# Optimization experiments

Measured on AMD Instinct MI355X. Metric: run time of the kernel, lower is better.

The kernel has to match this reference:

```python
import jax, jax.numpy as jnp
import numpy as np

ALPHA = 0.2  # LeakyReLU negative slope
NEG = -9e15

def _gat_head(Wh, a1, a2, adj_mask):
    # Wh: [N,O], a1/a2: [O], adj_mask: [N,N] bool
    e = jax.nn.leaky_relu(jnp.einsum('no,o->n', Wh, a1)[:, None]
                          + jnp.einsum('no,o->n', Wh, a2)[None, :], ALPHA)
    att = jax.nn.softmax(jnp.where(adj_mask, e, NEG), axis=-1)
    return att @ Wh  # [N,O]

def setup_inputs() -> dict:
    key = jax.random.key(0)
    ks = jax.random.split(key, 6)
    N, F_IN, O, H, C = 4096, 512, 64, 8, 16
    x = jax.random.normal(ks[0], (N, F_IN), jnp.float32)
    adj = jax.random.randint(ks[1], (N, N), 0, 2, jnp.int32)
    W = jax.random.normal(ks[2], (H, F_IN, O), jnp.float32) * 0.05
    a = jax.random.normal(ks[3], (H, 2 * O), jnp.float32) * 0.05
    W_out = jax.random.normal(ks[4], (H * O, C), jnp.float32) * 0.05
    a_out = jax.random.normal(ks[5], (2 * C,), jnp.float32) * 0.05
    return {'x': x, 'adj': adj, 'W': W, 'a': a, 'W_out': W_out, 'a_out': a_out}

def reference(x, adj, W, a, W_out, a_out):
    N = x.shape[0]
    H, _, O = W.shape
    C = W_out.shape[1]
    mask = adj > 0  # [N,N]
    # multi-head attention layer (vmapped over heads)
    Wh = jnp.einsum('nf,hfo->hno', x, W)  # [H,N,O]
    a1, a2 = a[:, :O], a[:, O:]
    h_heads = jax.vmap(_gat_head, in_axes=(0, 0, 0, None))(Wh, a1, a2, mask)  # [H,N,O]
    h = jax.nn.elu(h_heads)  # concat=True -> elu per head
    h = jnp.transpose(h, (1, 0, 2)).reshape(N, H * O)  # concat heads
    # output attention layer (concat=False)
    Wh_o = h @ W_out  # [N,C]
    out = _gat_head(Wh_o, a_out[:C], a_out[C:], mask)  # [N,C]
    out = jax.nn.elu(out)
    return jax.nn.log_softmax(out, axis=1)
```

## Files before the change

kernel.cpp:

```cpp
#include <hip/hip_runtime.h>


typedef _Float16 h2 __attribute__((ext_vector_type(2)));
typedef _Float16 half8 __attribute__((ext_vector_type(8)));
typedef __attribute__((ext_vector_type(4))) float f32x4;
typedef unsigned long long u64;
typedef unsigned short u16;
typedef unsigned int u32;

__device__ __forceinline__ u16 f2h(float f){
  union { _Float16 h; u16 u; } c; c.h = (_Float16)f; return c.u;
}
__device__ __forceinline__ h2 u2h2(u32 u){ union { u32 u; h2 h; } c; c.u = u; return c.h; }
__device__ __forceinline__ u32 h22u(h2 h){ union { u32 u; h2 h; } c; c.h = h; return c.u; }
__device__ __forceinline__ half8 pk2h8(uint4 v){ union { uint4 u; half8 h; } c; c.u = v; return c.h; }

__device__ __forceinline__ void async16(void* lds, const void* g){
  __builtin_amdgcn_global_load_lds((const __attribute__((address_space(1))) u32*)g,
                                   (__attribute__((address_space(3))) u32*)lds, 16, 0, 0);
}
__device__ __forceinline__ void async4(void* lds, const void* g){
  __builtin_amdgcn_global_load_lds((const __attribute__((address_space(1))) u32*)g,
                                   (__attribute__((address_space(3))) u32*)lds, 4, 0, 0);
}

__global__ __launch_bounds__(256) void k_wpack(const float* __restrict__ W,
                                               u16* __restrict__ Wb16){
  int t = blockIdx.x * 256 + threadIdx.x;
  int o   = t & 63;
  int fgb = (t >> 6) & 63;
  int h   = t >> 12;
  const float* src = W + ((size_t)h * 512 + fgb * 8) * 64 + o;
  u32 pk[4];
  #pragma unroll
  for (int p = 0; p < 4; ++p)
    pk[p] = (u32)f2h(src[(2 * p) * 64]) | ((u32)f2h(src[(2 * p + 1) * 64]) << 16);
  *(uint4*)(Wb16 + ((size_t)h * 4096 + fgb * 64 + o) * 8) = *(uint4*)pk;
}

__global__ __launch_bounds__(256) void k_gemm1(const float* __restrict__ x,
                                               const u16* __restrict__ Wb16,
                                               const float* __restrict__ av,
                                               const int* __restrict__ adj,
                                               u16* __restrict__ whB,
                                               u64* __restrict__ bits_t,
                                               float* __restrict__ r1,
                                               u16* __restrict__ e21h, u16* __restrict__ e202h){
  __shared__ u16 tr[4096];
  int h    = blockIdx.y;
  int bx   = blockIdx.x;
  int tid  = threadIdx.x;
  int lane = tid & 63;
  int wv   = tid >> 6;

  if (bx >= 64){
    int B = h * 64 + (bx - 64);
    int uid0 = B * 512 + wv * 128;
    for (int k = 0; k < 128; k += 8){
      int v[8];
      #pragma unroll
      for (int q = 0; q < 8; ++q){
        int uid = uid0 + k + q;
        v[q] = adj[(size_t)(uid >> 6) * 4096 + ((uid & 63) << 6) + lane];
      }
      u64 m[8];
      #pragma unroll
      for (int q = 0; q < 8; ++q) m[q] = __ballot(v[q] != 0);
      if (lane == 0){
        #pragma unroll
        for (int q = 0; q < 8; ++q){
          int uid = uid0 + k + q;
          bits_t[(size_t)(uid & 63) * 4096 + (uid >> 6)] = m[q];
        }
      }
    }
    return;
  }

  int row16 = lane & 15, grp = lane >> 4;
  int n0 = bx * 64;
  int n0w = n0 + wv * 16;
  const u16* wb = Wb16 + (size_t)h * 32768;

  f32x4 acc[4] = {};
  #pragma unroll 4
  for (int ks = 0; ks < 16; ++ks){
    int fgb = ks * 4 + grp;
    const float* xs = x + (size_t)(n0w + row16) * 512 + fgb * 8;
    float4 xv0 = ((const float4*)xs)[0];
    float4 xv1 = ((const float4*)xs)[1];
    u32 ax[4];
    ax[0] = (u32)f2h(xv0.x) | ((u32)f2h(xv0.y) << 16);
    ax[1] = (u32)f2h(xv0.z) | ((u32)f2h(xv0.w) << 16);
    ax[2] = (u32)f2h(xv1.x) | ((u32)f2h(xv1.y) << 16);
    ax[3] = (u32)f2h(xv1.z) | ((u32)f2h(xv1.w) << 16);
    half8 af = pk2h8(*(uint4*)ax);
    #pragma unroll
    for (int nt = 0; nt < 4; ++nt){
      half8 bf = *(const half8*)(wb + ((size_t)fgb * 64 + nt * 16 + row16) * 8);
      acc[nt] = __builtin_amdgcn_mfma_f32_16x16x32_f16(af, bf, acc[nt], 0, 0, 0);
    }
  }
  float a1v[4], a2v[4];
  #pragma unroll
  for (int nt = 0; nt < 4; ++nt){
    a1v[nt] = av[h * 128 + nt * 16 + row16];
    a2v[nt] = av[h * 128 + 64 + nt * 16 + row16];
  }
  #pragma unroll
  for (int r = 0; r < 4; ++r){
    float p1 = acc[0][r]*a1v[0] + acc[1][r]*a1v[1] + acc[2][r]*a1v[2] + acc[3][r]*a1v[3];
    float p2 = acc[0][r]*a2v[0] + acc[1][r]*a2v[1] + acc[2][r]*a2v[2] + acc[3][r]*a2v[3];
    #pragma unroll
    for (int d = 1; d < 16; d <<= 1){ p1 += __shfl_xor(p1, d, 64); p2 += __shfl_xor(p2, d, 64); }
    if (row16 == 0){
      int idx = h * 4096 + n0w + grp * 4 + r;
      r1[idx]    = __expf(-0.8f * p1);
      e21h[idx]  = f2h(__expf(p2));
      e202h[idx] = f2h(__expf(0.2f * p2));
    }
  }
  #pragma unroll
  for (int nt = 0; nt < 4; ++nt)
    #pragma unroll
    for (int r = 0; r < 4; ++r){
      int jl = wv * 16 + grp * 4 + r;
      int o  = nt * 16 + row16;
      tr[((jl >> 3) * 64 + o) * 8 + (jl & 7)] = f2h(acc[nt][r]);
    }
  __syncthreads();
  u16* dst = whB + (size_t)h * 262144 + (size_t)n0 * 64;
  #pragma unroll
  for (int q = 0; q < 2; ++q)
    *(uint4*)(dst + (tid * 2 + q) * 8) = *(const uint4*)(tr + (tid * 2 + q) * 8);
}

__global__ __launch_bounds__(256) void k_att1(const u16* __restrict__ whB,
                                              const u64* __restrict__ bits_t,
                                              const float* __restrict__ r1,
                                              const u16* __restrict__ e21h, const u16* __restrict__ e202h,
                                              u16* __restrict__ pnum, float* __restrict__ pden){
  __shared__ u16  smB[2][8192];
  __shared__ u32  smT[2][2][64];
  __shared__ u32  smLut[4];
  int h     = blockIdx.y;
  int iblk  = blockIdx.x;
  int split = blockIdx.z;
  int lane = threadIdx.x & 63;
  int wv   = threadIdx.x >> 6;
  int tid  = threadIdx.x;
  int row16 = lane & 15, grp = lane >> 4;
  if (threadIdx.x < 4)
    smLut[threadIdx.x] = ((threadIdx.x & 1) ? 0xFFFFu : 0u) | ((threadIdx.x & 2) ? 0xFFFF0000u : 0u);
  int i = iblk * 64 + wv * 16 + row16;
  int hoff = h * 4096;
  u32 rb = (u32)f2h(r1[hoff + i]); rb |= rb << 16;
  h2 rr = u2h2(rb);
  const u16* whBh = whB + (size_t)h * 262144;
  int jbeg = split * 1024;

  half8 bden;
  {
    u32 z[4] = {0,0,0,0};
    if (row16 == 0){ z[0]=0x3C003C00u; z[1]=0x3C003C00u; z[2]=0x3C003C00u; z[3]=0x3C003C00u; }
    bden = pk2h8(*(uint4*)z);
  }

  auto stage = [&](int bb, int j0){
    const char* g = (const char*)whBh + (size_t)j0 * 128 + tid * 16;
    char* l = (char*)(&smB[bb][0]) + tid * 16;
    #pragma unroll
    for (int k = 0; k < 4; ++k)
      async16(l + k * 4096, g + k * 4096);
    if (wv == 0)      async4(&smT[bb][0][0], (const char*)(e21h  + hoff + j0) + lane * 4);
    else if (wv == 1) async4(&smT[bb][1][0], (const char*)(e202h + hoff + j0) + lane * 4);
  };

  f32x4 acc[4] = {};
  f32x4 accden = {};
  stage(0, jbeg);
  for (int c = 0; c < 8; ++c){
    int bb = c & 1;
    u64 mrow0 = bits_t[(size_t)(split * 16 + c * 2)     * 4096 + i];
    u64 mrow1 = bits_t[(size_t)(split * 16 + c * 2 + 1) * 4096 + i];
    __syncthreads();
    if (c < 7) stage(bb ^ 1, jbeg + (c + 1) * 128);
    #pragma unroll
    for (int ks = 0; ks < 4; ++ks){
      uint4 e1q = *(const uint4*)((const char*)&smT[bb][0][0] + ks * 64 + grp * 16);
      uint4 e2q = *(const uint4*)((const char*)&smT[bb][1][0] + ks * 64 + grp * 16);
      u32 es[4] = {e1q.x, e1q.y, e1q.z, e1q.w};
      u32 gs[4] = {e2q.x, e2q.y, e2q.z, e2q.w};
      const u16* bbase = &smB[bb][(ks * 4 + grp) * 512];
      half8 bf0 = *(const half8*)(bbase + (0 * 16 + row16) * 8);
      half8 bf1 = *(const half8*)(bbase + (1 * 16 + row16) * 8);
      half8 bf2 = *(const half8*)(bbase + (2 * 16 + row16) * 8);
      half8 bf3 = *(const half8*)(bbase + (3 * 16 + row16) * 8);
      u64 mrow = (ks < 2) ? mrow0 : mrow1;
      u32 mb = ((u32)(mrow >> ((ks & 1) * 32)) >> (grp * 8)) & 0xffu;
      u32 pk[4];
      #pragma unroll
      for (int t2i = 0; t2i < 4; ++t2i){
        h2 w = __builtin_elementwise_max(u2h2(es[t2i]), rr * u2h2(gs[t2i]));
        pk[t2i] = h22u(w) & smLut[(mb >> (2 * t2i)) & 3u];
      }
      half8 af = pk2h8(*(uint4*)pk);
      acc[0] = __builtin_amdgcn_mfma_f32_16x16x32_f16(af, bf0, acc[0], 0, 0, 0);
      acc[1] = __builtin_amdgcn_mfma_f32_16x16x32_f16(af, bf1, acc[1], 0, 0, 0);
      acc[2] = __builtin_amdgcn_mfma_f32_16x16x32_f16(af, bf2, acc[2], 0, 0, 0);
      acc[3] = __builtin_amdgcn_mfma_f32_16x16x32_f16(af, bf3, acc[3], 0, 0, 0);
      accden = __builtin_amdgcn_mfma_f32_16x16x32_f16(af, bden, accden, 0, 0, 0);
    }
  }

  #pragma unroll
  for (int r4 = 0; r4 < 4; ++r4){
    int n = iblk * 64 + wv * 16 + grp * 4 + r4;
    if (row16 == 0)
      pden[((size_t)split * 8 + h) * 4096 + n] = accden[r4];
    u16* dst = pnum + ((size_t)split * 4096 + n) * 512 + h * 64 + row16;
    #pragma unroll
    for (int nt = 0; nt < 4; ++nt)
      dst[nt * 16] = f2h(acc[nt][r4]);
  }
}

__global__ __launch_bounds__(256) void k_gemm2(const u16* __restrict__ pnum,
                                               const float* __restrict__ pden,
                                               const float* __restrict__ Wout,
                                               const float* __restrict__ aout,
                                               u16* __restrict__ whoB,
                                               float* __restrict__ r1o,
                                               u16* __restrict__ e21oh, u16* __restrict__ e202oh){
  __shared__ float hrowf[4][512];
  int n0  = blockIdx.x * 4;
  int tid = threadIdx.x;
  {
    int nn = tid >> 6;
    int fc = tid & 63;
    int f0 = fc * 8;
    int hh = fc >> 3;
    int n  = n0 + nn;
    float v[8] = {0.f,0.f,0.f,0.f,0.f,0.f,0.f,0.f};
    float d = 0.f;
    #pragma unroll
    for (int s = 0; s < 4; ++s){
      uint4 raw = *(const uint4*)(pnum + ((size_t)s * 4096 + n) * 512 + f0);
      u32 rw[4] = {raw.x, raw.y, raw.z, raw.w};
      #pragma unroll
      for (int q = 0; q < 4; ++q){
        h2 dh = u2h2(rw[q]);
        v[q * 2]     += (float)dh.x;
        v[q * 2 + 1] += (float)dh.y;
      }
      d += pden[((size_t)s * 8 + hh) * 4096 + n];
    }
    float dinv = 1.f / d;
    #pragma unroll
    for (int k = 0; k < 8; ++k){
      float val = v[k] * dinv;
      hrowf[nn][f0 + k] = val > 0.f ? val : (__expf(val) - 1.f);
    }
  }
  __syncthreads();
  int rl = tid >> 6;
  int kq = (tid >> 4) & 3;
  int c  = tid & 15;
  int n  = n0 + rl;
  const float* hr = &hrowf[rl][kq * 128];
  const float* wp = Wout + (size_t)(kq * 128) * 16 + c;
  float a0 = 0.f, a1 = 0.f;
  #pragma unroll 16
  for (int f = 0; f < 128; f += 2){
    a0 += hr[f]     * wp[f * 16];
    a1 += hr[f + 1] * wp[f * 16 + 16];
  }
  float acc = a0 + a1;
  acc += __shfl_xor(acc, 16, 64);
  acc += __shfl_xor(acc, 32, 64);
  int lane = tid & 63;
  if ((lane >> 4) == 0)
    whoB[((size_t)(n >> 3) * 16 + c) * 8 + (n & 7)] = f2h(acc);
  float p1 = acc * aout[c], p2 = acc * aout[16 + c];
  #pragma unroll
  for (int d = 1; d < 16; d <<= 1){ p1 += __shfl_xor(p1, d, 64); p2 += __shfl_xor(p2, d, 64); }
  if (lane == 0){
    r1o[n]    = __expf(-0.8f * p1);
    e21oh[n]  = f2h(__expf(p2));
    e202oh[n] = f2h(__expf(0.2f * p2));
  }
}

__global__ __launch_bounds__(256) void k_att2(const u16* __restrict__ whoB,
                                              const u64* __restrict__ bits_t,
                                              const float* __restrict__ r1o,
                                              const u16* __restrict__ e21oh, const u16* __restrict__ e202oh,
                                              float* __restrict__ pnum, float* __restrict__ pden){
  __shared__ u32 smLut[4];
  int iblk  = blockIdx.x;
  int split = blockIdx.y;
  int lane = threadIdx.x & 63;
  int wv   = threadIdx.x >> 6;
  int row16 = lane & 15, grp = lane >> 4;
  if (threadIdx.x < 4)
    smLut[threadIdx.x] = ((threadIdx.x & 1) ? 0xFFFFu : 0u) | ((threadIdx.x & 2) ? 0xFFFF0000u : 0u);
  __syncthreads();
  int i = iblk * 64 + wv * 16 + row16;
  u32 rb = (u32)f2h(r1o[i]); rb |= rb << 16;
  h2 rr = u2h2(rb);
  int jbeg = split * 256;
  half8 bden;
  {
    u32 z[4] = {0,0,0,0};
    if (row16 == 0){ z[0]=0x3C003C00u; z[1]=0x3C003C00u; z[2]=0x3C003C00u; z[3]=0x3C003C00u; }
    bden = pk2h8(*(uint4*)z);
  }

  f32x4 acc = {};
  f32x4 accden = {};
  #pragma unroll
  for (int c = 0; c < 4; ++c){
    int j0 = jbeg + c * 64;
    u64 mrow = bits_t[(size_t)(split * 4 + c) * 4096 + i];
    #pragma unroll
    for (int ks = 0; ks < 2; ++ks){
      int sb = (j0 >> 3) + ks * 4 + grp;
      half8 bf = *(const half8*)(whoB + ((size_t)sb * 16 + row16) * 8);
      uint4 e1q = *(const uint4*)(e21oh  + j0 + ks * 32 + grp * 8);
      uint4 e2q = *(const uint4*)(e202oh + j0 + ks * 32 + grp * 8);
      u32 es[4] = {e1q.x, e1q.y, e1q.z, e1q.w};
      u32 gs[4] = {e2q.x, e2q.y, e2q.z, e2q.w};
      u32 mb = ((u32)(mrow >> (ks * 32)) >> (grp * 8)) & 0xffu;
      u32 pk[4];
      #pragma unroll
      for (int t2i = 0; t2i < 4; ++t2i){
        h2 w = __builtin_elementwise_max(u2h2(es[t2i]), rr * u2h2(gs[t2i]));
        pk[t2i] = h22u(w) & smLut[(mb >> (2 * t2i)) & 3u];
      }
      half8 af = pk2h8(*(uint4*)pk);
      acc    = __builtin_amdgcn_mfma_f32_16x16x32_f16(af, bf, acc, 0, 0, 0);
      accden = __builtin_amdgcn_mfma_f32_16x16x32_f16(af, bden, accden, 0, 0, 0);
    }
  }
  #pragma unroll
  for (int r4 = 0; r4 < 4; ++r4){
    int n = iblk * 64 + wv * 16 + grp * 4 + r4;
    if (row16 == 0)
      pden[(size_t)n * 16 + split] = accden[r4];
    pnum[((size_t)n * 16 + split) * 16 + row16] = acc[r4];
  }
}

__global__ __launch_bounds__(256) void k_final(const float* __restrict__ pnum,
                                               const float* __restrict__ pden,
                                               float* __restrict__ out){
  int tid = blockIdx.x * 256 + threadIdx.x;
  int c = tid & 15;
  int n = tid >> 4;
  float num = 0.f, den = 0.f;
  #pragma unroll
  for (int s = 0; s < 16; ++s){
    num += pnum[((size_t)n * 16 + s) * 16 + c];
    den += pden[(size_t)n * 16 + s];
  }
  float v = num / den;
  v = v > 0.f ? v : (__expf(v) - 1.f);
  float m = v;
  #pragma unroll
  for (int d = 1; d < 16; d <<= 1) m = fmaxf(m, __shfl_xor(m, d, 64));
  float es = __expf(v - m), ss = es;
  #pragma unroll
  for (int d = 1; d < 16; d <<= 1) ss += __shfl_xor(ss, d, 64);
  out[(size_t)n * 16 + c] = v - m - __logf(ss);
}

extern "C" void kernel_launch(void* const* d_in, const int* in_sizes, int n_in,
                              void* d_out, int out_size, void* d_ws, size_t ws_size,
                              hipStream_t stream){
  (void)in_sizes; (void)n_in; (void)out_size; (void)ws_size;
  const float* x    = (const float*)d_in[0];
  const int*   adj  = (const int*)d_in[1];
  const float* W    = (const float*)d_in[2];
  const float* av   = (const float*)d_in[3];
  const float* Wout = (const float*)d_in[4];
  const float* aout = (const float*)d_in[5];
  float* out = (float*)d_out;
  char* ws = (char*)d_ws;

  u64*  bits_t  = (u64*)(ws + 0x0000000);
  u16*  whB     = (u16*)(ws + 0x0200000);
  float* r1     = (float*)(ws + 0x0600000);
  u16*  e21h    = (u16*)(ws + 0x0620000);
  u16*  e202h   = (u16*)(ws + 0x0630000);
  u16*  pnum1   = (u16*)(ws + 0x0680000);
  float* pden1  = (float*)(ws + 0x1680000);
  u16*  whoB    = (u16*)(ws + 0x1700000);
  float* r1o    = (float*)(ws + 0x1720000);
  u16*  e21oh   = (u16*)(ws + 0x1724000);
  u16*  e202oh  = (u16*)(ws + 0x1726000);
  float* pnum2  = (float*)(ws + 0x1730000);
  float* pden2  = (float*)(ws + 0x1B30000);
  u16*  Wb16    = (u16*)(ws + 0x1730000);

  k_wpack<<<dim3(128), dim3(256), 0, stream>>>(W, Wb16);
  k_gemm1<<<dim3(128, 8), dim3(256), 0, stream>>>(x, Wb16, av, adj, whB, bits_t, r1, e21h, e202h);
  k_att1<<<dim3(64, 8, 4), dim3(256), 0, stream>>>(whB, bits_t, r1, e21h, e202h, pnum1, pden1);
  k_gemm2<<<dim3(1024), dim3(256), 0, stream>>>(pnum1, pden1, Wout, aout, whoB, r1o, e21oh, e202oh);
  k_att2<<<dim3(64, 16), dim3(256), 0, stream>>>(whoB, bits_t, r1o, e21oh, e202oh, pnum2, pden2);
  k_final<<<dim3(256), dim3(256), 0, stream>>>(pnum2, pden2, out);
}
```

Measured before the change: 170.1 us.

## Fuse output attention with final softmax and spread adjacency packing across more blocks

```diff
diff --git a/kernel.cpp b/kernel.cpp
--- a/kernel.cpp
+++ b/kernel.cpp
@@ -54,9 +54,9 @@
   int wv   = tid >> 6;
 
   if (bx >= 64){
-    int B = h * 64 + (bx - 64);
-    int uid0 = B * 512 + wv * 128;
-    for (int k = 0; k < 128; k += 8){
+    int B2 = h * 256 + (bx - 64);
+    int uid0 = B2 * 128 + wv * 32;
+    for (int k = 0; k < 32; k += 8){
       int v[8];
       #pragma unroll
       for (int q = 0; q < 8; ++q){
@@ -291,24 +291,25 @@
   }
 }
 
-__global__ __launch_bounds__(256) void k_att2(const u16* __restrict__ whoB,
-                                              const u64* __restrict__ bits_t,
-                                              const float* __restrict__ r1o,
-                                              const u16* __restrict__ e21oh, const u16* __restrict__ e202oh,
-                                              float* __restrict__ pnum, float* __restrict__ pden){
+__global__ __launch_bounds__(256) void k_att2f(const u16* __restrict__ whoB,
+                                               const u64* __restrict__ bits_t,
+                                               const float* __restrict__ r1o,
+                                               const u16* __restrict__ e21oh, const u16* __restrict__ e202oh,
+                                               float* __restrict__ out){
   __shared__ u32 smLut[4];
-  int iblk  = blockIdx.x;
-  int split = blockIdx.y;
-  int lane = threadIdx.x & 63;
-  int wv   = threadIdx.x >> 6;
+  __shared__ float rnum[4][256];
+  __shared__ float rden[4][16];
+  int iblk = blockIdx.x;
+  int tid  = threadIdx.x;
+  int lane = tid & 63;
+  int wv   = tid >> 6;
   int row16 = lane & 15, grp = lane >> 4;
-  if (threadIdx.x < 4)
-    smLut[threadIdx.x] = ((threadIdx.x & 1) ? 0xFFFFu : 0u) | ((threadIdx.x & 2) ? 0xFFFF0000u : 0u);
+  if (tid < 4)
+    smLut[tid] = ((tid & 1) ? 0xFFFFu : 0u) | ((tid & 2) ? 0xFFFF0000u : 0u);
   __syncthreads();
-  int i = iblk * 64 + wv * 16 + row16;
+  int i = iblk * 16 + row16;
   u32 rb = (u32)f2h(r1o[i]); rb |= rb << 16;
   h2 rr = u2h2(rb);
-  int jbeg = split * 256;
   half8 bden;
   {
     u32 z[4] = {0,0,0,0};
@@ -318,10 +319,10 @@
 
   f32x4 acc = {};
   f32x4 accden = {};
-  #pragma unroll
-  for (int c = 0; c < 4; ++c){
-    int j0 = jbeg + c * 64;
-    u64 mrow = bits_t[(size_t)(split * 4 + c) * 4096 + i];
+  for (int k = 0; k < 16; ++k){
+    int chunk = wv * 16 + k;
+    int j0 = chunk * 64;
+    u64 mrow = bits_t[(size_t)chunk * 4096 + i];
     #pragma unroll
     for (int ks = 0; ks < 2; ++ks){
       int sb = (j0 >> 3) + ks * 4 + grp;
@@ -344,25 +345,14 @@
   }
   #pragma unroll
   for (int r4 = 0; r4 < 4; ++r4){
-    int n = iblk * 64 + wv * 16 + grp * 4 + r4;
-    if (row16 == 0)
-      pden[(size_t)n * 16 + split] = accden[r4];
-    pnum[((size_t)n * 16 + split) * 16 + row16] = acc[r4];
-  }
-}
-
-__global__ __launch_bounds__(256) void k_final(const float* __restrict__ pnum,
-                                               const float* __restrict__ pden,
-                                               float* __restrict__ out){
-  int tid = blockIdx.x * 256 + threadIdx.x;
-  int c = tid & 15;
-  int n = tid >> 4;
-  float num = 0.f, den = 0.f;
-  #pragma unroll
-  for (int s = 0; s < 16; ++s){
-    num += pnum[((size_t)n * 16 + s) * 16 + c];
-    den += pden[(size_t)n * 16 + s];
-  }
+    rnum[wv][(grp * 4 + r4) * 16 + row16] = acc[r4];
+    if (row16 == 0) rden[wv][grp * 4 + r4] = accden[r4];
+  }
+  __syncthreads();
+  int r = tid >> 4, c = tid & 15;
+  float num = rnum[0][r * 16 + c] + rnum[1][r * 16 + c]
+            + rnum[2][r * 16 + c] + rnum[3][r * 16 + c];
+  float den = rden[0][r] + rden[1][r] + rden[2][r] + rden[3][r];
   float v = num / den;
   v = v > 0.f ? v : (__expf(v) - 1.f);
   float m = v;
@@ -371,7 +361,7 @@
   float es = __expf(v - m), ss = es;
   #pragma unroll
   for (int d = 1; d < 16; d <<= 1) ss += __shfl_xor(ss, d, 64);
-  out[(size_t)n * 16 + c] = v - m - __logf(ss);
+  out[(size_t)(iblk * 16 + r) * 16 + c] = v - m - __logf(ss);
 }
 
 extern "C" void kernel_launch(void* const* d_in, const int* in_sizes, int n_in,
@@ -398,14 +388,11 @@
   float* r1o    = (float*)(ws + 0x1720000);
   u16*  e21oh   = (u16*)(ws + 0x1724000);
   u16*  e202oh  = (u16*)(ws + 0x1726000);
-  float* pnum2  = (float*)(ws + 0x1730000);
-  float* pden2  = (float*)(ws + 0x1B30000);
   u16*  Wb16    = (u16*)(ws + 0x1730000);
 
   k_wpack<<<dim3(128), dim3(256), 0, stream>>>(W, Wb16);
-  k_gemm1<<<dim3(128, 8), dim3(256), 0, stream>>>(x, Wb16, av, adj, whB, bits_t, r1, e21h, e202h);
+  k_gemm1<<<dim3(320, 8), dim3(256), 0, stream>>>(x, Wb16, av, adj, whB, bits_t, r1, e21h, e202h);
   k_att1<<<dim3(64, 8, 4), dim3(256), 0, stream>>>(whB, bits_t, r1, e21h, e202h, pnum1, pden1);
   k_gemm2<<<dim3(1024), dim3(256), 0, stream>>>(pnum1, pden1, Wout, aout, whoB, r1o, e21oh, e202oh);
-  k_att2<<<dim3(64, 16), dim3(256), 0, stream>>>(whoB, bits_t, r1o, e21oh, e202oh, pnum2, pden2);
-  k_final<<<dim3(256), dim3(256), 0, stream>>>(pnum2, pden2, out);
-}
+  k_att2f<<<dim3(256), dim3(256), 0, stream>>>(whoB, bits_t, r1o, e21oh, e202oh, out);
+}
```

New measurement: 182.5 us. 7.3% more time.

## Overlap next-tile async loads with the barrier and coalesce pnum stores through LDS

Applied to the files above, without the earlier changes.

```diff
diff --git a/kernel.cpp b/kernel.cpp
--- a/kernel.cpp
+++ b/kernel.cpp
@@ -146,12 +146,12 @@
   int h     = blockIdx.y;
   int iblk  = blockIdx.x;
   int split = blockIdx.z;
-  int lane = threadIdx.x & 63;
-  int wv   = threadIdx.x >> 6;
   int tid  = threadIdx.x;
+  int lane = tid & 63;
+  int wv   = tid >> 6;
   int row16 = lane & 15, grp = lane >> 4;
-  if (threadIdx.x < 4)
-    smLut[threadIdx.x] = ((threadIdx.x & 1) ? 0xFFFFu : 0u) | ((threadIdx.x & 2) ? 0xFFFF0000u : 0u);
+  if (tid < 4)
+    smLut[tid] = ((tid & 1) ? 0xFFFFu : 0u) | ((tid & 2) ? 0xFFFF0000u : 0u);
   int i = iblk * 64 + wv * 16 + row16;
   int hoff = h * 4096;
   u32 rb = (u32)f2h(r1[hoff + i]); rb |= rb << 16;
@@ -172,8 +172,9 @@
     #pragma unroll
     for (int k = 0; k < 4; ++k)
       async16(l + k * 4096, g + k * 4096);
-    if (wv == 0)      async4(&smT[bb][0][0], (const char*)(e21h  + hoff + j0) + lane * 4);
-    else if (wv == 1) async4(&smT[bb][1][0], (const char*)(e202h + hoff + j0) + lane * 4);
+    int tsel = wv & 1;
+    const u16* tb = tsel ? e202h : e21h;
+    async4(&smT[bb][tsel][0], (const char*)(tb + hoff + j0) + lane * 4);
   };
 
   f32x4 acc[4] = {};
@@ -183,8 +184,13 @@
     int bb = c & 1;
     u64 mrow0 = bits_t[(size_t)(split * 16 + c * 2)     * 4096 + i];
     u64 mrow1 = bits_t[(size_t)(split * 16 + c * 2 + 1) * 4096 + i];
-    __syncthreads();
-    if (c < 7) stage(bb ^ 1, jbeg + (c + 1) * 128);
+    if (c < 7){
+      stage(bb ^ 1, jbeg + (c + 1) * 128);
+      asm volatile("s_waitcnt vmcnt(5)" ::: "memory");
+    } else {
+      asm volatile("s_waitcnt vmcnt(0)" ::: "memory");
+    }
+    __builtin_amdgcn_s_barrier();
     #pragma unroll
     for (int ks = 0; ks < 4; ++ks){
       uint4 e1q = *(const uint4*)((const char*)&smT[bb][0][0] + ks * 64 + grp * 16);
@@ -218,10 +224,24 @@
     int n = iblk * 64 + wv * 16 + grp * 4 + r4;
     if (row16 == 0)
       pden[((size_t)split * 8 + h) * 4096 + n] = accden[r4];
-    u16* dst = pnum + ((size_t)split * 4096 + n) * 512 + h * 64 + row16;
-    #pragma unroll
-    for (int nt = 0; nt < 4; ++nt)
-      dst[nt * 16] = f2h(acc[nt][r4]);
+  }
+  u16* trn = (u16*)&smB[0][0];
+  #pragma unroll
+  for (int nt = 0; nt < 4; ++nt)
+    #pragma unroll
+    for (int r4 = 0; r4 < 4; ++r4){
+      int nl = wv * 16 + grp * 4 + r4;
+      trn[nl * 72 + nt * 16 + row16] = f2h(acc[nt][r4]);
+    }
+  __syncthreads();
+  {
+    int rl = tid >> 2;
+    int q  = tid & 3;
+    int n  = iblk * 64 + rl;
+    const uint4* src = (const uint4*)(trn + rl * 72 + q * 16);
+    u16* dst = pnum + ((size_t)split * 4096 + n) * 512 + h * 64 + q * 16;
+    ((uint4*)dst)[0] = src[0];
+    ((uint4*)dst)[1] = src[1];
   }
 }
 
```

Result: slower. 174.2 us (+2.4%).
